# Optimization experiments

Measured on AMD Instinct MI355X. Metric: run time of the kernel, lower is better.

## Reference

```python
import jax, jax.numpy as jnp
import numpy as np

HEADS = 8
DIM_HEAD = 64
SCALE = DIM_HEAD ** -0.5


def setup_inputs() -> dict:
    key = jax.random.key(0)
    ks = jax.random.split(key, 5)
    B, N, M, D = 8, 1024, 1024, 512
    inner = HEADS * DIM_HEAD  # 512
    return {
        "x": jax.random.normal(ks[0], (B, N, D), dtype=jnp.float32),
        "context": jax.random.normal(ks[1], (B, M, D), dtype=jnp.float32),
        "Wq": jax.random.normal(ks[2], (D, inner), dtype=jnp.float32) * (D ** -0.5),
        "Wkv": jax.random.normal(ks[3], (D, 2 * inner), dtype=jnp.float32) * (D ** -0.5),
        "Wo": jax.random.normal(ks[4], (inner, D), dtype=jnp.float32) * (inner ** -0.5),
        "bo": jnp.zeros((D,), dtype=jnp.float32),
    }


def reference(x, context, Wq, Wkv, Wo, bo):
    B, N, D = x.shape
    M = context.shape[1]
    q = x @ Wq                      # [B, N, inner]
    kv = context @ Wkv              # [B, M, 2*inner]
    k, v = jnp.split(kv, 2, axis=-1)
    # b n (h d) -> b h n d
    split_heads = lambda t: t.reshape(t.shape[0], t.shape[1], HEADS, DIM_HEAD).transpose(0, 2, 1, 3)
    q, k, v = split_heads(q), split_heads(k), split_heads(v)
    dots = jnp.einsum('bhid,bhjd->bhij', q, k) * SCALE  # [B, H, N, M]
    attn = jax.nn.softmax(dots, axis=-1)
    out = jnp.einsum('bhij,bhjd->bhid', attn, v)        # [B, H, N, d]
    out = out.transpose(0, 2, 1, 3).reshape(B, N, HEADS * DIM_HEAD)
    return out @ Wo + bo            # [B, N, D]
```

## Files before the change

kernel.cpp:

```cpp
#include <hip/hip_runtime.h>
#include <stdint.h>

#define LOG2E 1.44269504088896340736f
#define QSCALE (0.125f * LOG2E)

typedef __bf16 bf16x8 __attribute__((ext_vector_type(8)));
typedef float floatx4 __attribute__((ext_vector_type(4)));

__device__ __forceinline__ unsigned short bfbits(float f) {
  __bf16 h = (__bf16)f;
  return __builtin_bit_cast(unsigned short, h);
}

__device__ __forceinline__ float fast_exp2(float x) {
#if __has_builtin(__builtin_amdgcn_exp2f)
  return __builtin_amdgcn_exp2f(x);
#else
  return exp2f(x);
#endif
}

__device__ __forceinline__ void gl2lds16(const void* g, void* l) {
  __builtin_amdgcn_global_load_lds((const __attribute__((address_space(1))) void*)g,
                                   (__attribute__((address_space(3))) void*)l, 16, 0, 0);
}

__global__ __launch_bounds__(256)
void prep_kernel(const float* __restrict__ x, const float* __restrict__ ctx,
                 const float* __restrict__ Wq, const float* __restrict__ Wkv,
                 const float* __restrict__ Wo,
                 unsigned short* __restrict__ Xb, unsigned short* __restrict__ Cb,
                 unsigned short* __restrict__ WqT, unsigned short* __restrict__ WkvT,
                 unsigned short* __restrict__ WoT) {
  int blk = blockIdx.x;
  int tid = threadIdx.x;
  if (blk < 8192) {
    const float* in = blk < 4096 ? x : ctx;
    unsigned short* out = blk < 4096 ? Xb : Cb;
    int i = (((blk & 4095) * 256) + tid) * 4;
    float4 v = *(const float4*)(in + i);
    unsigned long long pk = (unsigned long long)bfbits(v.x)
                          | ((unsigned long long)bfbits(v.y) << 16)
                          | ((unsigned long long)bfbits(v.z) << 32)
                          | ((unsigned long long)bfbits(v.w) << 48);
    *(unsigned long long*)(out + i) = pk;
  } else {
    __shared__ float tile[32][33];
    int t = blk - 8192;
    const float* in; unsigned short* out; int N; int tb;
    if (t < 256)      { in = Wq;  out = WqT;  N = 512;  tb = t; }
    else if (t < 768) { in = Wkv; out = WkvT; N = 1024; tb = t - 256; }
    else              { in = Wo;  out = WoT;  N = 512;  tb = t - 768; }
    const int K = 512;
    int nbx = N / 32;
    int n0 = (tb % nbx) * 32, k0 = (tb / nbx) * 32;
    int tx = tid & 31, ty = tid >> 5;
#pragma unroll
    for (int r = ty; r < 32; r += 8)
      tile[r][tx] = in[(long)(k0 + r) * N + n0 + tx];
    __syncthreads();
#pragma unroll
    for (int r = ty; r < 32; r += 8)
      out[(long)(n0 + r) * K + k0 + tx] = bfbits(tile[tx][r]);
  }
}

__global__ __launch_bounds__(256)
void proj_gemm(const unsigned short* __restrict__ Xb, const unsigned short* __restrict__ Cb,
               const unsigned short* __restrict__ WqT, const unsigned short* __restrict__ WkvT,
               unsigned short* __restrict__ Qb, unsigned short* __restrict__ Kb,
               unsigned short* __restrict__ Vt) {
  __shared__ unsigned short As[128 * 64];
  __shared__ unsigned short Bs[128 * 64];

  int idx0 = blockIdx.x;
  int idx = (idx0 & 7) * 96 + (idx0 >> 3);
  const unsigned short* A; const unsigned short* Bt;
  long bm, bn; int role;
  if (idx < 256) { role = 0; A = Xb; Bt = WqT;  bn = (long)(idx & 3) * 128; bm = (long)(idx >> 2) * 128; }
  else { int j = idx - 256; role = 1; A = Cb; Bt = WkvT; bn = (long)(j & 7) * 128; bm = (long)(j >> 3) * 128; }

  const int tid = threadIdx.x;
  const int wave = tid >> 6;
  const int lane = tid & 63;
  const int l15 = lane & 15;
  const int q4 = lane >> 4;
  const int s7 = l15 & 7;
  const int wm = (wave & 1) * 64;
  const int wn = (wave >> 1) * 64;
  const int K = 512;

  int aoff[4], boff[4], lds16[4];
#pragma unroll
  for (int cc = 0; cc < 4; ++cc) {
    int c = cc * 256 + tid;
    int r = c >> 3, kc = c & 7;
    int sw = (kc ^ (r & 7)) * 8;
    aoff[cc] = (int)(bm + r) * K + sw;
    boff[cc] = (int)(bn + r) * K + sw;
    lds16[cc] = c * 16;
  }
  int arow[4], brow[4], csw[2];
#pragma unroll
  for (int i = 0; i < 4; ++i) {
    arow[i] = (wm + i * 16 + l15) * 64;
    brow[i] = (wn + i * 16 + l15) * 64;
  }
#pragma unroll
  for (int ks = 0; ks < 2; ++ks) csw[ks] = ((ks * 4 + q4) ^ s7) * 8;

  floatx4 acc[4][4];
#pragma unroll
  for (int i = 0; i < 4; ++i)
#pragma unroll
    for (int j = 0; j < 4; ++j) { acc[i][j][0]=0.f; acc[i][j][1]=0.f; acc[i][j][2]=0.f; acc[i][j][3]=0.f; }

  for (int k0 = 0; k0 < K; k0 += 64) {
#pragma unroll
    for (int cc = 0; cc < 4; ++cc) {
      gl2lds16(A + aoff[cc] + k0, (char*)As + lds16[cc]);
      gl2lds16(Bt + boff[cc] + k0, (char*)Bs + lds16[cc]);
    }
    __syncthreads();
#pragma unroll
    for (int ks = 0; ks < 2; ++ks) {
      bf16x8 af[4], bfr[4];
#pragma unroll
      for (int i = 0; i < 4; ++i) af[i] = *(const bf16x8*)(As + arow[i] + csw[ks]);
#pragma unroll
      for (int j = 0; j < 4; ++j) bfr[j] = *(const bf16x8*)(Bs + brow[j] + csw[ks]);
#pragma unroll
      for (int i = 0; i < 4; ++i)
#pragma unroll
        for (int j = 0; j < 4; ++j)
          acc[i][j] = __builtin_amdgcn_mfma_f32_16x16x32_bf16(af[i], bfr[j], acc[i][j], 0, 0, 0);
    }
    __syncthreads();
  }

  const bool vrole = (role == 1) && (bn >= 512);
#pragma unroll
  for (int i = 0; i < 4; ++i) {
#pragma unroll
    for (int j = 0; j < 4; ++j) {
      long col = bn + wn + j * 16 + l15;
      if (vrole) {
        long h = (col - 512) >> 6, d = col & 63;
        long row0 = bm + wm + i * 16 + q4 * 4;
        long b = row0 >> 10, m0 = row0 & 1023;
        unsigned long long pk = (unsigned long long)bfbits(acc[i][j][0])
                              | ((unsigned long long)bfbits(acc[i][j][1]) << 16)
                              | ((unsigned long long)bfbits(acc[i][j][2]) << 32)
                              | ((unsigned long long)bfbits(acc[i][j][3]) << 48);
        *(unsigned long long*)(Vt + ((b * 8 + h) * 64 + d) * 1024 + m0) = pk;
      } else {
        long h = col >> 6, d = col & 63;
#pragma unroll
        for (int r = 0; r < 4; ++r) {
          long row = bm + wm + i * 16 + q4 * 4 + r;
          long b = row >> 10, n = row & 1023;
          float v = acc[i][j][r];
          if (role == 0) Qb[((b * 8 + h) * 1024 + n) * 64 + d] = bfbits(v * QSCALE);
          else           Kb[((b * 8 + h) * 1024 + n) * 64 + d] = bfbits(v);
        }
      }
    }
  }
}

__global__ __launch_bounds__(256)
void attn_kernel(const unsigned short* __restrict__ Qb,
                 const unsigned short* __restrict__ Kb,
                 const unsigned short* __restrict__ Vt,
                 unsigned short* __restrict__ Ob)
{
  __shared__ unsigned short Ksm[2][4096];
  __shared__ unsigned short Vsm[2][4096];
  __shared__ unsigned short Psm[128 * 64];

  const int tid = threadIdx.x;
  const int wave = tid >> 6;
  const int lane = tid & 63;
  const int l15 = lane & 15;
  const int q4 = lane >> 4;
  const int bh = blockIdx.x;
  const int nb = blockIdx.y;

  const long qrow0 = (long)bh * 1024 + nb * 128 + wave * 32;

  bf16x8 qf[2][2];
#pragma unroll
  for (int qn = 0; qn < 2; ++qn)
#pragma unroll
    for (int ks = 0; ks < 2; ++ks)
      qf[qn][ks] = *(const bf16x8*)(Qb + (qrow0 + qn * 16 + l15) * 64 + ks * 32 + q4 * 8);

  floatx4 acc[2][4];
#pragma unroll
  for (int i = 0; i < 2; ++i)
#pragma unroll
    for (int d = 0; d < 4; ++d) { acc[i][d][0]=0.f; acc[i][d][1]=0.f; acc[i][d][2]=0.f; acc[i][d][3]=0.f; }
  float suml[2] = {0.0f, 0.0f};

  const unsigned short* Kbase = Kb + (long)bh * 65536;
  const unsigned short* Vbase = Vt + (long)bh * 65536;
  int koff[2], voff[2], lds16[2];
#pragma unroll
  for (int cc = 0; cc < 2; ++cc) {
    int c = cc * 256 + tid;
    int jrow = c >> 3;
    int cact = (c & 7) ^ (jrow & 7);
    koff[cc] = jrow * 64 + cact * 8;
    voff[cc] = jrow * 1024 + cact * 8;
    lds16[cc] = c * 16;
  }

  const int s7 = l15 & 7;
  int kfo[2][4];
  int pao[2][2];
  int pwo[2][4];
#pragma unroll
  for (int ks = 0; ks < 2; ++ks) {
#pragma unroll
    for (int jn = 0; jn < 4; ++jn)
      kfo[ks][jn] = (jn * 16 + l15) * 64 + (((ks * 4 + q4) ^ s7) * 8);
#pragma unroll
    for (int i = 0; i < 2; ++i)
      pao[ks][i] = (wave * 32 + i * 16 + l15) * 64 + (((ks * 4 + q4) ^ s7) * 8);
  }
#pragma unroll
  for (int qn = 0; qn < 2; ++qn)
#pragma unroll
    for (int jn = 0; jn < 4; ++jn)
      pwo[qn][jn] = (wave * 32 + qn * 16 + l15) * 64 + (((jn * 2 + (q4 >> 1)) ^ s7) * 8) + (q4 & 1) * 4;

#pragma unroll
  for (int cc = 0; cc < 2; ++cc) {
    gl2lds16(Kbase + koff[cc], (char*)Ksm[0] + lds16[cc]);
    gl2lds16(Vbase + voff[cc], (char*)Vsm[0] + lds16[cc]);
  }

#define ATTN_TILE(TIDX, CUR, STAGE)                                                          \
  {                                                                                          \
    __syncthreads();                                                                         \
    if (STAGE) {                                                                             \
      _Pragma("unroll")                                                                      \
      for (int cc = 0; cc < 2; ++cc) {                                                       \
        gl2lds16(Kbase + ((TIDX) + 1) * 4096 + koff[cc], (char*)Ksm[(CUR) ^ 1] + lds16[cc]); \
        gl2lds16(Vbase + ((TIDX) + 1) * 64 + voff[cc], (char*)Vsm[(CUR) ^ 1] + lds16[cc]);   \
      }                                                                                      \
    }                                                                                        \
    floatx4 st[4][2];                                                                        \
    _Pragma("unroll")                                                                        \
    for (int jn = 0; jn < 4; ++jn)                                                           \
      _Pragma("unroll")                                                                      \
      for (int qn = 0; qn < 2; ++qn) {                                                       \
        st[jn][qn][0] = 0.f; st[jn][qn][1] = 0.f; st[jn][qn][2] = 0.f; st[jn][qn][3] = 0.f;  \
      }                                                                                      \
    _Pragma("unroll")                                                                        \
    for (int ks = 0; ks < 2; ++ks) {                                                         \
      bf16x8 kfr[4];                                                                         \
      _Pragma("unroll")                                                                      \
      for (int jn = 0; jn < 4; ++jn)                                                         \
        kfr[jn] = *(const bf16x8*)(Ksm[(CUR)] + kfo[ks][jn]);                                \
      __builtin_amdgcn_s_setprio(1);                                                         \
      _Pragma("unroll")                                                                      \
      for (int jn = 0; jn < 4; ++jn)                                                         \
        _Pragma("unroll")                                                                    \
        for (int qn = 0; qn < 2; ++qn)                                                       \
          st[jn][qn] = __builtin_amdgcn_mfma_f32_16x16x32_bf16(kfr[jn], qf[qn][ks],          \
                                                               st[jn][qn], 0, 0, 0);         \
      __builtin_amdgcn_s_setprio(0);                                                         \
    }                                                                                        \
    bf16x8 vbt[2][4];        \
    _Pragma("unroll")                                                                        \
    for (int ks = 0; ks < 2; ++ks)                                                           \
      _Pragma("unroll")                                                                      \
      for (int dn = 0; dn < 4; ++dn)                                                         \
        vbt[ks][dn] = *(const bf16x8*)(Vsm[(CUR)] + kfo[ks][dn]);                            \
    _Pragma("unroll")                                                                        \
    for (int qn = 0; qn < 2; ++qn) {                                                         \
      _Pragma("unroll")                                                                      \
      for (int jn = 0; jn < 4; ++jn) {                                                       \
        float p0 = fast_exp2(st[jn][qn][0]);                                                 \
        float p1 = fast_exp2(st[jn][qn][1]);                                                 \
        float p2 = fast_exp2(st[jn][qn][2]);                                                 \
        float p3 = fast_exp2(st[jn][qn][3]);                                                 \
        suml[qn] += (p0 + p1) + (p2 + p3);                                                   \
        unsigned int lo = (unsigned int)bfbits(p0) | ((unsigned int)bfbits(p1) << 16);       \
        unsigned int hi = (unsigned int)bfbits(p2) | ((unsigned int)bfbits(p3) << 16);       \
        unsigned long long pk = (unsigned long long)lo | ((unsigned long long)hi << 32);     \
        *(unsigned long long*)(Psm + pwo[qn][jn]) = pk;                                      \
      }                                                                                      \
    }                                                                                        \
    __asm__ volatile("s_waitcnt lgkmcnt(0)" ::: "memory");                                   \
    _Pragma("unroll")                                                                        \
    for (int ks = 0; ks < 2; ++ks) {                                                         \
      bf16x8 pa[2];                                                                          \
      _Pragma("unroll")                                                                      \
      for (int i = 0; i < 2; ++i)                                                            \
        pa[i] = *(const bf16x8*)(Psm + pao[ks][i]);                                          \
      __builtin_amdgcn_s_setprio(1);                                                         \
      _Pragma("unroll")                                                                      \
      for (int i = 0; i < 2; ++i)                                                            \
        _Pragma("unroll")                                                                    \
        for (int dn = 0; dn < 4; ++dn)                                                       \
          acc[i][dn] = __builtin_amdgcn_mfma_f32_16x16x32_bf16(pa[i], vbt[ks][dn],           \
                                                               acc[i][dn], 0, 0, 0);         \
      __builtin_amdgcn_s_setprio(0);                                                         \
    }                                                                                        \
  }

  for (int tt = 0; tt < 8; ++tt) {
    ATTN_TILE(2 * tt, 0, true);
    ATTN_TILE(2 * tt + 1, 1, (tt < 7));
  }
#undef ATTN_TILE

  float inv[2], invr[2][4];
#pragma unroll
  for (int qn = 0; qn < 2; ++qn) {
    float l = suml[qn];
    l += __shfl_xor(l, 16, 64);
    l += __shfl_xor(l, 32, 64);
    inv[qn] = 1.0f / l;
#pragma unroll
    for (int r = 0; r < 4; ++r) invr[qn][r] = __shfl(inv[qn], q4 * 4 + r, 64);
  }

  const int b = bh >> 3, h = bh & 7;
#pragma unroll
  for (int i = 0; i < 2; ++i) {
#pragma unroll
    for (int dn = 0; dn < 4; ++dn) {
#pragma unroll
      for (int r = 0; r < 4; ++r) {
        long row = (long)b * 1024 + nb * 128 + wave * 32 + i * 16 + q4 * 4 + r;
        long col = h * 64 + dn * 16 + l15;
        Ob[row * 512 + col] = bfbits(acc[i][dn][r] * invr[i][r]);
      }
    }
  }
}

__global__ __launch_bounds__(256)
void out_gemm(const unsigned short* __restrict__ A,
              const unsigned short* __restrict__ Bt,
              float* __restrict__ outF, const float* __restrict__ bias) {
  __shared__ unsigned short As[64 * 64];
  __shared__ unsigned short Bs[128 * 64];

  int bid = blockIdx.x;
  int swz = (bid & 7) * 64 + (bid >> 3);
  const long bm = (long)(swz >> 2) * 64;
  const long bn = (long)(swz & 3) * 128;

  const int tid = threadIdx.x;
  const int wave = tid >> 6;
  const int lane = tid & 63;
  const int l15 = lane & 15;
  const int q4 = lane >> 4;
  const int s7 = l15 & 7;
  const int wm = (wave & 1) * 32;
  const int wn = (wave >> 1) * 64;
  const int K = 512, N = 512;

  int aoff[2], boff[4], alds[2], blds[4];
#pragma unroll
  for (int cc = 0; cc < 2; ++cc) {
    int c = cc * 256 + tid;
    int r = c >> 3, kc = c & 7;
    aoff[cc] = (int)(bm + r) * K + (kc ^ (r & 7)) * 8;
    alds[cc] = c * 16;
  }
#pragma unroll
  for (int cc = 0; cc < 4; ++cc) {
    int c = cc * 256 + tid;
    int r = c >> 3, kc = c & 7;
    boff[cc] = (int)(bn + r) * K + (kc ^ (r & 7)) * 8;
    blds[cc] = c * 16;
  }
  int arow[2], brow[4], csw[2];
#pragma unroll
  for (int i = 0; i < 2; ++i) arow[i] = (wm + i * 16 + l15) * 64;
#pragma unroll
  for (int j = 0; j < 4; ++j) brow[j] = (wn + j * 16 + l15) * 64;
#pragma unroll
  for (int ks = 0; ks < 2; ++ks) csw[ks] = ((ks * 4 + q4) ^ s7) * 8;

  floatx4 acc[2][4];
#pragma unroll
  for (int i = 0; i < 2; ++i)
#pragma unroll
    for (int j = 0; j < 4; ++j) { acc[i][j][0]=0.f; acc[i][j][1]=0.f; acc[i][j][2]=0.f; acc[i][j][3]=0.f; }

  for (int k0 = 0; k0 < K; k0 += 64) {
#pragma unroll
    for (int cc = 0; cc < 2; ++cc)
      gl2lds16(A + aoff[cc] + k0, (char*)As + alds[cc]);
#pragma unroll
    for (int cc = 0; cc < 4; ++cc)
      gl2lds16(Bt + boff[cc] + k0, (char*)Bs + blds[cc]);
    __syncthreads();
#pragma unroll
    for (int ks = 0; ks < 2; ++ks) {
      bf16x8 af[2], bfr[4];
#pragma unroll
      for (int i = 0; i < 2; ++i) af[i] = *(const bf16x8*)(As + arow[i] + csw[ks]);
#pragma unroll
      for (int j = 0; j < 4; ++j) bfr[j] = *(const bf16x8*)(Bs + brow[j] + csw[ks]);
#pragma unroll
      for (int i = 0; i < 2; ++i)
#pragma unroll
        for (int j = 0; j < 4; ++j)
          acc[i][j] = __builtin_amdgcn_mfma_f32_16x16x32_bf16(af[i], bfr[j], acc[i][j], 0, 0, 0);
    }
    __syncthreads();
  }

#pragma unroll
  for (int i = 0; i < 2; ++i) {
#pragma unroll
    for (int j = 0; j < 4; ++j) {
      long col = bn + wn + j * 16 + l15;
      float bv = bias[col];
#pragma unroll
      for (int r = 0; r < 4; ++r) {
        long row = bm + wm + i * 16 + q4 * 4 + r;
        outF[row * (long)N + col] = acc[i][j][r] + bv;
      }
    }
  }
}

extern "C" void kernel_launch(void* const* d_in, const int* in_sizes, int n_in,
                              void* d_out, int out_size, void* d_ws, size_t ws_size,
                              hipStream_t stream) {
  const float* x   = (const float*)d_in[0];
  const float* ctx = (const float*)d_in[1];
  const float* Wq  = (const float*)d_in[2];
  const float* Wkv = (const float*)d_in[3];
  const float* Wo  = (const float*)d_in[4];
  const float* bo  = (const float*)d_in[5];
  float* out = (float*)d_out;

  char* ws = (char*)d_ws;
  unsigned short* Xb   = (unsigned short*)(ws);
  unsigned short* Cb   = (unsigned short*)(ws + (8u  << 20));
  unsigned short* WqT  = (unsigned short*)(ws + (16u << 20));
  unsigned short* WkvT = (unsigned short*)(ws + (17u << 20));
  unsigned short* WoT  = (unsigned short*)(ws + (19u << 20));
  unsigned short* Qb   = (unsigned short*)(ws + (20u << 20));
  unsigned short* Kb   = (unsigned short*)(ws + (28u << 20));
  unsigned short* Vt   = (unsigned short*)(ws + (36u << 20));
  unsigned short* Ob   = (unsigned short*)(ws + (44u << 20));

  prep_kernel<<<9216, 256, 0, stream>>>(x, ctx, Wq, Wkv, Wo, Xb, Cb, WqT, WkvT, WoT);
  proj_gemm<<<768, 256, 0, stream>>>(Xb, Cb, WqT, WkvT, Qb, Kb, Vt);
  attn_kernel<<<dim3(64, 8), 256, 0, stream>>>(Qb, Kb, Vt, Ob);
  out_gemm<<<512, 256, 0, stream>>>(Ob, WoT, out, bo);
}
```

Measured before the change: 155.1 us.

## Halve attention and output-GEMM tile sizes to double block count

The attention kernel now gives each block 64 query rows (16 per wave) instead of 128, launching 1024 blocks with an XCD-aware block index remap. The output GEMM moves from 64x128 to 64x64 tiles, also launching 1024 blocks. The aim is to fill all compute units on a 256-CU device, since 512 blocks left CUs underused. The cost is that K/V tiles are reloaded twice as often per query row, and each wave issues fewer MFMAs per LDS read, which lowers arithmetic intensity.

```diff
diff --git a/kernel.cpp b/kernel.cpp
--- a/kernel.cpp
+++ b/kernel.cpp
@@ -176,31 +176,29 @@
 {
   __shared__ unsigned short Ksm[2][4096];
   __shared__ unsigned short Vsm[2][4096];
-  __shared__ unsigned short Psm[128 * 64];
+  __shared__ unsigned short Psm[64 * 64];
 
   const int tid = threadIdx.x;
   const int wave = tid >> 6;
   const int lane = tid & 63;
   const int l15 = lane & 15;
   const int q4 = lane >> 4;
-  const int bh = blockIdx.x;
-  const int nb = blockIdx.y;
-
-  const long qrow0 = (long)bh * 1024 + nb * 128 + wave * 32;
-
-  bf16x8 qf[2][2];
-#pragma unroll
-  for (int qn = 0; qn < 2; ++qn)
-#pragma unroll
-    for (int ks = 0; ks < 2; ++ks)
-      qf[qn][ks] = *(const bf16x8*)(Qb + (qrow0 + qn * 16 + l15) * 64 + ks * 32 + q4 * 8);
-
-  floatx4 acc[2][4];
-#pragma unroll
-  for (int i = 0; i < 2; ++i)
-#pragma unroll
-    for (int d = 0; d < 4; ++d) { acc[i][d][0]=0.f; acc[i][d][1]=0.f; acc[i][d][2]=0.f; acc[i][d][3]=0.f; }
-  float suml[2] = {0.0f, 0.0f};
+  const int bid = blockIdx.x;
+  const int lin = (bid & 7) * 128 + (bid >> 3);
+  const int bh = lin >> 4;
+  const int nb = lin & 15;
+
+  const long qrow0 = (long)bh * 1024 + nb * 64 + wave * 16;
+
+  bf16x8 qf[2];
+#pragma unroll
+  for (int ks = 0; ks < 2; ++ks)
+    qf[ks] = *(const bf16x8*)(Qb + (qrow0 + l15) * 64 + ks * 32 + q4 * 8);
+
+  floatx4 acc[4];
+#pragma unroll
+  for (int d = 0; d < 4; ++d) { acc[d][0]=0.f; acc[d][1]=0.f; acc[d][2]=0.f; acc[d][3]=0.f; }
+  float suml = 0.0f;
 
   const unsigned short* Kbase = Kb + (long)bh * 65536;
   const unsigned short* Vbase = Vt + (long)bh * 65536;
@@ -217,22 +215,18 @@
 
   const int s7 = l15 & 7;
   int kfo[2][4];
-  int pao[2][2];
-  int pwo[2][4];
+  int pao[2];
+  int pwo[4];
 #pragma unroll
   for (int ks = 0; ks < 2; ++ks) {
 #pragma unroll
     for (int jn = 0; jn < 4; ++jn)
       kfo[ks][jn] = (jn * 16 + l15) * 64 + (((ks * 4 + q4) ^ s7) * 8);
-#pragma unroll
-    for (int i = 0; i < 2; ++i)
-      pao[ks][i] = (wave * 32 + i * 16 + l15) * 64 + (((ks * 4 + q4) ^ s7) * 8);
-  }
-#pragma unroll
-  for (int qn = 0; qn < 2; ++qn)
-#pragma unroll
-    for (int jn = 0; jn < 4; ++jn)
-      pwo[qn][jn] = (wave * 32 + qn * 16 + l15) * 64 + (((jn * 2 + (q4 >> 1)) ^ s7) * 8) + (q4 & 1) * 4;
+    pao[ks] = (wave * 16 + l15) * 64 + (((ks * 4 + q4) ^ s7) * 8);
+  }
+#pragma unroll
+  for (int jn = 0; jn < 4; ++jn)
+    pwo[jn] = (wave * 16 + l15) * 64 + (((jn * 2 + (q4 >> 1)) ^ s7) * 8) + (q4 & 1) * 4;
 
 #pragma unroll
   for (int cc = 0; cc < 2; ++cc) {
@@ -250,13 +244,11 @@
         gl2lds16(Vbase + ((TIDX) + 1) * 64 + voff[cc], (char*)Vsm[(CUR) ^ 1] + lds16[cc]);   \
       }                                                                                      \
     }                                                                                        \
-    floatx4 st[4][2];                                                                        \
+    floatx4 st[4];                                                                           \
     _Pragma("unroll")                                                                        \
-    for (int jn = 0; jn < 4; ++jn)                                                           \
-      _Pragma("unroll")                                                                      \
-      for (int qn = 0; qn < 2; ++qn) {                                                       \
-        st[jn][qn][0] = 0.f; st[jn][qn][1] = 0.f; st[jn][qn][2] = 0.f; st[jn][qn][3] = 0.f;  \
-      }                                                                                      \
+    for (int jn = 0; jn < 4; ++jn) {                                                         \
+      st[jn][0] = 0.f; st[jn][1] = 0.f; st[jn][2] = 0.f; st[jn][3] = 0.f;                    \
+    }                                                                                        \
     _Pragma("unroll")                                                                        \
     for (int ks = 0; ks < 2; ++ks) {                                                         \
       bf16x8 kfr[4];                                                                         \
@@ -266,10 +258,7 @@
       __builtin_amdgcn_s_setprio(1);                                                         \
       _Pragma("unroll")                                                                      \
       for (int jn = 0; jn < 4; ++jn)                                                         \
-        _Pragma("unroll")                                                                    \
-        for (int qn = 0; qn < 2; ++qn)                                                       \
-          st[jn][qn] = __builtin_amdgcn_mfma_f32_16x16x32_bf16(kfr[jn], qf[qn][ks],          \
-                                                               st[jn][qn], 0, 0, 0);         \
+        st[jn] = __builtin_amdgcn_mfma_f32_16x16x32_bf16(kfr[jn], qf[ks], st[jn], 0, 0, 0);  \
       __builtin_amdgcn_s_setprio(0);                                                         \
     }                                                                                        \
     bf16x8 vbt[2][4];        \
@@ -279,34 +268,25 @@
       for (int dn = 0; dn < 4; ++dn)                                                         \
         vbt[ks][dn] = *(const bf16x8*)(Vsm[(CUR)] + kfo[ks][dn]);                            \
     _Pragma("unroll")                                                                        \
-    for (int qn = 0; qn < 2; ++qn) {                                                         \
-      _Pragma("unroll")                                                                      \
-      for (int jn = 0; jn < 4; ++jn) {                                                       \
-        float p0 = fast_exp2(st[jn][qn][0]);                                                 \
-        float p1 = fast_exp2(st[jn][qn][1]);                                                 \
-        float p2 = fast_exp2(st[jn][qn][2]);                                                 \
-        float p3 = fast_exp2(st[jn][qn][3]);                                                 \
-        suml[qn] += (p0 + p1) + (p2 + p3);                                                   \
-        unsigned int lo = (unsigned int)bfbits(p0) | ((unsigned int)bfbits(p1) << 16);       \
-        unsigned int hi = (unsigned int)bfbits(p2) | ((unsigned int)bfbits(p3) << 16);       \
-        unsigned long long pk = (unsigned long long)lo | ((unsigned long long)hi << 32);     \
-        *(unsigned long long*)(Psm + pwo[qn][jn]) = pk;                                      \
-      }                                                                                      \
+    for (int jn = 0; jn < 4; ++jn) {                                                         \
+      float p0 = fast_exp2(st[jn][0]);                                                       \
+      float p1 = fast_exp2(st[jn][1]);                                                       \
+      float p2 = fast_exp2(st[jn][2]);                                                       \
+      float p3 = fast_exp2(st[jn][3]);                                                       \
+      suml += (p0 + p1) + (p2 + p3);                                                         \
+      unsigned int lo = (unsigned int)bfbits(p0) | ((unsigned int)bfbits(p1) << 16);         \
+      unsigned int hi = (unsigned int)bfbits(p2) | ((unsigned int)bfbits(p3) << 16);         \
+      unsigned long long pk = (unsigned long long)lo | ((unsigned long long)hi << 32);       \
+      *(unsigned long long*)(Psm + pwo[jn]) = pk;                                            \
     }                                                                                        \
     __asm__ volatile("s_waitcnt lgkmcnt(0)" ::: "memory");                                   \
     _Pragma("unroll")                                                                        \
     for (int ks = 0; ks < 2; ++ks) {                                                         \
-      bf16x8 pa[2];                                                                          \
-      _Pragma("unroll")                                                                      \
-      for (int i = 0; i < 2; ++i)                                                            \
-        pa[i] = *(const bf16x8*)(Psm + pao[ks][i]);                                          \
+      bf16x8 pa = *(const bf16x8*)(Psm + pao[ks]);                                           \
       __builtin_amdgcn_s_setprio(1);                                                         \
       _Pragma("unroll")                                                                      \
-      for (int i = 0; i < 2; ++i)                                                            \
-        _Pragma("unroll")                                                                    \
-        for (int dn = 0; dn < 4; ++dn)                                                       \
-          acc[i][dn] = __builtin_amdgcn_mfma_f32_16x16x32_bf16(pa[i], vbt[ks][dn],           \
-                                                               acc[i][dn], 0, 0, 0);         \
+      for (int dn = 0; dn < 4; ++dn)                                                         \
+        acc[dn] = __builtin_amdgcn_mfma_f32_16x16x32_bf16(pa, vbt[ks][dn], acc[dn], 0, 0, 0);\
       __builtin_amdgcn_s_setprio(0);                                                         \
     }                                                                                        \
   }
@@ -317,28 +297,22 @@
   }
 #undef ATTN_TILE
 
-  float inv[2], invr[2][4];
-#pragma unroll
-  for (int qn = 0; qn < 2; ++qn) {
-    float l = suml[qn];
-    l += __shfl_xor(l, 16, 64);
-    l += __shfl_xor(l, 32, 64);
-    inv[qn] = 1.0f / l;
-#pragma unroll
-    for (int r = 0; r < 4; ++r) invr[qn][r] = __shfl(inv[qn], q4 * 4 + r, 64);
-  }
+  float l = suml;
+  l += __shfl_xor(l, 16, 64);
+  l += __shfl_xor(l, 32, 64);
+  float inv = 1.0f / l;
+  float invr[4];
+#pragma unroll
+  for (int r = 0; r < 4; ++r) invr[r] = __shfl(inv, q4 * 4 + r, 64);
 
   const int b = bh >> 3, h = bh & 7;
 #pragma unroll
-  for (int i = 0; i < 2; ++i) {
-#pragma unroll
-    for (int dn = 0; dn < 4; ++dn) {
-#pragma unroll
-      for (int r = 0; r < 4; ++r) {
-        long row = (long)b * 1024 + nb * 128 + wave * 32 + i * 16 + q4 * 4 + r;
-        long col = h * 64 + dn * 16 + l15;
-        Ob[row * 512 + col] = bfbits(acc[i][dn][r] * invr[i][r]);
-      }
+  for (int dn = 0; dn < 4; ++dn) {
+#pragma unroll
+    for (int r = 0; r < 4; ++r) {
+      long row = (long)b * 1024 + nb * 64 + wave * 16 + q4 * 4 + r;
+      long col = h * 64 + dn * 16 + l15;
+      Ob[row * 512 + col] = bfbits(acc[dn][r] * invr[r]);
     }
   }
 }
@@ -348,12 +322,12 @@
               const unsigned short* __restrict__ Bt,
               float* __restrict__ outF, const float* __restrict__ bias) {
   __shared__ unsigned short As[64 * 64];
-  __shared__ unsigned short Bs[128 * 64];
+  __shared__ unsigned short Bs[64 * 64];
 
   int bid = blockIdx.x;
-  int swz = (bid & 7) * 64 + (bid >> 3);
-  const long bm = (long)(swz >> 2) * 64;
-  const long bn = (long)(swz & 3) * 128;
+  int swz = (bid & 7) * 128 + (bid >> 3);
+  const long bm = (long)(swz >> 3) * 64;
+  const long bn = (long)(swz & 7) * 64;
 
   const int tid = threadIdx.x;
   const int wave = tid >> 6;
@@ -362,57 +336,52 @@
   const int q4 = lane >> 4;
   const int s7 = l15 & 7;
   const int wm = (wave & 1) * 32;
-  const int wn = (wave >> 1) * 64;
+  const int wn = (wave >> 1) * 32;
   const int K = 512, N = 512;
 
-  int aoff[2], boff[4], alds[2], blds[4];
+  int aoff[2], boff[2], lds16[2];
 #pragma unroll
   for (int cc = 0; cc < 2; ++cc) {
     int c = cc * 256 + tid;
     int r = c >> 3, kc = c & 7;
-    aoff[cc] = (int)(bm + r) * K + (kc ^ (r & 7)) * 8;
-    alds[cc] = c * 16;
-  }
-#pragma unroll
-  for (int cc = 0; cc < 4; ++cc) {
-    int c = cc * 256 + tid;
-    int r = c >> 3, kc = c & 7;
-    boff[cc] = (int)(bn + r) * K + (kc ^ (r & 7)) * 8;
-    blds[cc] = c * 16;
-  }
-  int arow[2], brow[4], csw[2];
-#pragma unroll
-  for (int i = 0; i < 2; ++i) arow[i] = (wm + i * 16 + l15) * 64;
-#pragma unroll
-  for (int j = 0; j < 4; ++j) brow[j] = (wn + j * 16 + l15) * 64;
+    int sw = (kc ^ (r & 7)) * 8;
+    aoff[cc] = (int)(bm + r) * K + sw;
+    boff[cc] = (int)(bn + r) * K + sw;
+    lds16[cc] = c * 16;
+  }
+  int arow[2], brow[2], csw[2];
+#pragma unroll
+  for (int i = 0; i < 2; ++i) {
+    arow[i] = (wm + i * 16 + l15) * 64;
+    brow[i] = (wn + i * 16 + l15) * 64;
+  }
 #pragma unroll
   for (int ks = 0; ks < 2; ++ks) csw[ks] = ((ks * 4 + q4) ^ s7) * 8;
 
-  floatx4 acc[2][4];
+  floatx4 acc[2][2];
 #pragma unroll
   for (int i = 0; i < 2; ++i)
 #pragma unroll
-    for (int j = 0; j < 4; ++j) { acc[i][j][0]=0.f; acc[i][j][1]=0.f; acc[i][j][2]=0.f; acc[i][j][3]=0.f; }
+    for (int j = 0; j < 2; ++j) { acc[i][j][0]=0.f; acc[i][j][1]=0.f; acc[i][j][2]=0.f; acc[i][j][3]=0.f; }
 
   for (int k0 = 0; k0 < K; k0 += 64) {
 #pragma unroll
-    for (int cc = 0; cc < 2; ++cc)
-      gl2lds16(A + aoff[cc] + k0, (char*)As + alds[cc]);
-#pragma unroll
-    for (int cc = 0; cc < 4; ++cc)
-      gl2lds16(Bt + boff[cc] + k0, (char*)Bs + blds[cc]);
+    for (int cc = 0; cc < 2; ++cc) {
+      gl2lds16(A + aoff[cc] + k0, (char*)As + lds16[cc]);
+      gl2lds16(Bt + boff[cc] + k0, (char*)Bs + lds16[cc]);
+    }
     __syncthreads();
 #pragma unroll
     for (int ks = 0; ks < 2; ++ks) {
-      bf16x8 af[2], bfr[4];
+      bf16x8 af[2], bfr[2];
 #pragma unroll
       for (int i = 0; i < 2; ++i) af[i] = *(const bf16x8*)(As + arow[i] + csw[ks]);
 #pragma unroll
-      for (int j = 0; j < 4; ++j) bfr[j] = *(const bf16x8*)(Bs + brow[j] + csw[ks]);
+      for (int j = 0; j < 2; ++j) bfr[j] = *(const bf16x8*)(Bs + brow[j] + csw[ks]);
 #pragma unroll
       for (int i = 0; i < 2; ++i)
 #pragma unroll
-        for (int j = 0; j < 4; ++j)
+        for (int j = 0; j < 2; ++j)
           acc[i][j] = __builtin_amdgcn_mfma_f32_16x16x32_bf16(af[i], bfr[j], acc[i][j], 0, 0, 0);
     }
     __syncthreads();
@@ -421,7 +390,7 @@
 #pragma unroll
   for (int i = 0; i < 2; ++i) {
 #pragma unroll
-    for (int j = 0; j < 4; ++j) {
+    for (int j = 0; j < 2; ++j) {
       long col = bn + wn + j * 16 + l15;
       float bv = bias[col];
 #pragma unroll
@@ -457,6 +426,6 @@
 
   prep_kernel<<<9216, 256, 0, stream>>>(x, ctx, Wq, Wkv, Wo, Xb, Cb, WqT, WkvT, WoT);
   proj_gemm<<<768, 256, 0, stream>>>(Xb, Cb, WqT, WkvT, Qb, Kb, Vt);
-  attn_kernel<<<dim3(64, 8), 256, 0, stream>>>(Qb, Kb, Vt, Ob);
-  out_gemm<<<512, 256, 0, stream>>>(Ob, WoT, out, bo);
-}
+  attn_kernel<<<1024, 256, 0, stream>>>(Qb, Kb, Vt, Ob);
+  out_gemm<<<1024, 256, 0, stream>>>(Ob, WoT, out, bo);
+}
```

Measured after the change: 162.4 us. 1.05x slower.
